# Performance work log

Measured on AMD Instinct MI355X. Metric: run time of the kernel, lower is better.

## Reference

```python
import jax, jax.numpy as jnp
import numpy as np

B, S, DIN, DOUT = 2, 2048, 4096, 4096


def setup_inputs() -> dict:
    key = jax.random.key(0)
    k1, k2 = jax.random.split(key)
    x = jax.random.normal(k1, (B, S, DIN), dtype=jnp.float32)
    weight = jax.random.normal(k2, (DOUT, DIN), dtype=jnp.float32) * 0.02
    # xnor init for row scaling pattern
    mean = weight.mean(-1, keepdims=True)                      # [DOUT,1]
    scale = jnp.abs(weight - mean).mean(-1, keepdims=True)     # [DOUT,1]
    wscale = scale
    wbias = mean
    return {"x": x, "weight": weight, "wscale": wscale, "wbias": wbias}


def reference(x, weight, wscale, wbias):
    # STE binarization: forward = sign(weight) (grad handled in bwd module)
    w_bin = jnp.sign(weight)
    w = wscale * w_bin + wbias                                 # [DOUT, DIN]
    # F.linear(x, w): x @ w.T, no bias
    out = jnp.einsum('bsk,nk->bsn', x, w)
    return out
```

## Files before the change

kernel.cpp:

```cpp
#include <hip/hip_runtime.h>
#include <stdint.h>


#define MDIM 4096
#define NDIM 4096
#define KDIM 4096

typedef int int4v  __attribute__((ext_vector_type(4)));

__device__ __forceinline__ int pack4_rn(float a, float b, float c, float d, float inv) {
  int ia = __float2int_rn(a * inv) & 0xff;
  int ib = __float2int_rn(b * inv) & 0xff;
  int ic = __float2int_rn(c * inv) & 0xff;
  int id = __float2int_rn(d * inv) & 0xff;
  return ia | (ib << 8) | (ic << 16) | (id << 24);
}

__device__ __forceinline__ int sgn8(float v) {
  return (v > 0.f) ? 1 : ((v < 0.f) ? 0xff : 0);
}

#define PREP_XB 1024
#define PREP_WB 1024
__global__ __launch_bounds__(256) void prep_kernel(
    const float* __restrict__ x, const float* __restrict__ w,
    char* __restrict__ xq, char* __restrict__ wsg,
    float* __restrict__ xscale, float* __restrict__ sumx) {
  const int b = blockIdx.x;
  const int tid = threadIdx.x;
  const int lane = tid & 63, wv = tid >> 6;
  if (b < PREP_XB) {
    const int row = b * 4 + wv;
    const float4* xr = (const float4*)(x + (size_t)row * KDIM);
    float4 v[16];
    float s = 0.f, amax = 0.f;
#pragma unroll
    for (int u = 0; u < 16; ++u) {
      v[u] = xr[u * 64 + lane];
      s += v[u].x + v[u].y + v[u].z + v[u].w;
      amax = fmaxf(amax, fmaxf(fmaxf(fabsf(v[u].x), fabsf(v[u].y)),
                               fmaxf(fabsf(v[u].z), fabsf(v[u].w))));
    }
#pragma unroll
    for (int off = 32; off > 0; off >>= 1) {
      s += __shfl_xor(s, off, 64);
      amax = fmaxf(amax, __shfl_xor(amax, off, 64));
    }
    if (lane == 0) {
      sumx[row] = s;
      xscale[row] = amax * (1.f / 127.f);
    }
    const float inv = (amax > 0.f) ? 127.f / amax : 0.f;
    int* xo = (int*)(xq + (size_t)row * KDIM);
#pragma unroll
    for (int u = 0; u < 16; ++u)
      xo[u * 64 + lane] = pack4_rn(v[u].x, v[u].y, v[u].z, v[u].w, inv);
  } else {
    const float4* wr = (const float4*)w;
    int* wo = (int*)wsg;
    const size_t i0 = (size_t)(b - PREP_XB) * 256 + tid;
    const size_t stride = (size_t)PREP_WB * 256;
#pragma unroll
    for (int u = 0; u < 16; ++u) {
      size_t i = i0 + (size_t)u * stride;
      float4 vv = wr[i];
      wo[i] = sgn8(vv.x) | (sgn8(vv.y) << 8) | (sgn8(vv.z) << 16) | (sgn8(vv.w) << 24);
    }
  }
}

__global__ __launch_bounds__(512, 2) void gemm_bin_i8_pipe(
    const char* __restrict__ A, const char* __restrict__ Bs,
    const float* __restrict__ wscale, const float* __restrict__ wbias,
    const float* __restrict__ xscale, const float* __restrict__ sumx,
    float* __restrict__ C) {
  __shared__ __align__(16) char sm[131072];

  const int bm = blockIdx.x >> 4, bn = blockIdx.x & 15;
  const int tm0 = bm * 256, tn0 = bn * 256;
  const int tid = threadIdx.x;
  const int lane = tid & 63, wave = tid >> 6;
  const int col32 = lane & 31, hl = lane >> 5;
  const int wr = wave >> 2, wc = wave & 3;

  typedef int int16v __attribute__((ext_vector_type(16)));
  int16v acc[4][2];
#pragma unroll
  for (int mi = 0; mi < 4; ++mi)
#pragma unroll
    for (int nj = 0; nj < 2; ++nj)
#pragma unroll
      for (int r = 0; r < 16; ++r) acc[mi][nj][r] = 0;

  int4v afA[4], bqA[2], afB[4], bqB[2];

  int aOff[2][4], bOff[2][2];
#pragma unroll
  for (int ks2 = 0; ks2 < 2; ++ks2) {
#pragma unroll
    for (int mi = 0; mi < 4; ++mi) {
      int row = wr * 128 + mi * 32 + col32;
      int sw = (row >> 1) & 3;
      aOff[ks2][mi] = row * 64 + (((ks2 * 2 + hl) ^ sw) & 3) * 16;
    }
#pragma unroll
    for (int nj = 0; nj < 2; ++nj) {
      int row = wc * 64 + nj * 32 + col32;
      int sw = (row >> 1) & 3;
      bOff[ks2][nj] = 65536 + row * 64 + (((ks2 * 2 + hl) ^ sw) & 3) * 16;
    }
  }

  const int u0 = tid, u1 = tid + 512;
  const int r0 = u0 >> 2, r1 = u1 >> 2;
  const int c0 = (u0 & 3) ^ ((r0 >> 1) & 3);
  const int c1 = (u1 & 3) ^ ((r1 >> 1) & 3);
  const char* gA0 = A + (size_t)(tm0 + r0) * KDIM + c0 * 16;
  const char* gA1 = A + (size_t)(tm0 + r1) * KDIM + c1 * 16;
  const char* gB0 = Bs + (size_t)(tn0 + r0) * KDIM + c0 * 16;
  const char* gB1 = Bs + (size_t)(tn0 + r1) * KDIM + c1 * 16;
  const int ldsu0 = tid * 16, ldsu1 = 8192 + tid * 16;

#define STAGE_A(BUF, KH, KOFS)                                                    \
  do {                                                                            \
    const int base_ = ((BUF) * 2 + (KH)) * 16384;                                 \
    __builtin_amdgcn_global_load_lds(                                             \
        (const __attribute__((address_space(1))) void*)(gA0 + (KOFS)),            \
        (__attribute__((address_space(3))) void*)(sm + base_ + ldsu0), 16, 0, 0); \
    __builtin_amdgcn_global_load_lds(                                             \
        (const __attribute__((address_space(1))) void*)(gA1 + (KOFS)),            \
        (__attribute__((address_space(3))) void*)(sm + base_ + ldsu1), 16, 0, 0); \
  } while (0)

#define STAGE_B(BUF, KH, KOFS)                                                    \
  do {                                                                            \
    const int base_ = 65536 + ((BUF) * 2 + (KH)) * 16384;                         \
    __builtin_amdgcn_global_load_lds(                                             \
        (const __attribute__((address_space(1))) void*)(gB0 + (KOFS)),            \
        (__attribute__((address_space(3))) void*)(sm + base_ + ldsu0), 16, 0, 0); \
    __builtin_amdgcn_global_load_lds(                                             \
        (const __attribute__((address_space(1))) void*)(gB1 + (KOFS)),            \
        (__attribute__((address_space(3))) void*)(sm + base_ + ldsu1), 16, 0, 0); \
  } while (0)

#define DSRD(SET, BUF, KS, KS2)                                                   \
  do {                                                                            \
    _Pragma("unroll") for (int mi_ = 0; mi_ < 4; ++mi_)                           \
        af##SET[mi_] =                                                            \
            *(const int4v*)(sm + ((BUF) * 2 + (KS)) * 16384 + aOff[KS2][mi_]);    \
    _Pragma("unroll") for (int nj_ = 0; nj_ < 2; ++nj_)                           \
        bq##SET[nj_] =                                                            \
            *(const int4v*)(sm + ((BUF) * 2 + (KS)) * 16384 + bOff[KS2][nj_]);    \
  } while (0)

#define MFMA8(SET)                                                                \
  do {                                                                            \
    __builtin_amdgcn_s_setprio(1);                                                \
    _Pragma("unroll") for (int mi_ = 0; mi_ < 4; ++mi_)                           \
        _Pragma("unroll") for (int nj_ = 0; nj_ < 2; ++nj_)                       \
            acc[mi_][nj_] = __builtin_amdgcn_mfma_i32_32x32x32_i8(                \
                af##SET[mi_], bq##SET[nj_], acc[mi_][nj_], 0, 0, 0);              \
    __builtin_amdgcn_s_setprio(0);                                                \
  } while (0)

#define WAITL6                                                                    \
  do {                                                                            \
    asm volatile("s_waitcnt lgkmcnt(6)" ::: "memory");                            \
    __builtin_amdgcn_sched_barrier(0);                                            \
  } while (0)
#define WAITL0                                                                    \
  do {                                                                            \
    asm volatile("s_waitcnt lgkmcnt(0)" ::: "memory");                            \
    __builtin_amdgcn_sched_barrier(0);                                            \
  } while (0)

#define BARO __builtin_amdgcn_s_barrier()
#define CK6  asm volatile("s_waitcnt vmcnt(6)\n\ts_barrier" ::: "memory")
#define CK4  asm volatile("s_waitcnt vmcnt(4)\n\ts_barrier" ::: "memory")
#define CK0  asm volatile("s_waitcnt vmcnt(0)\n\ts_barrier" ::: "memory")

#define PHASEP(CSET, NSET, NBUF, NKS, NKS2, STAGEOP, ENDSYNC)                     \
  do {                                                                            \
    DSRD(NSET, NBUF, NKS, NKS2);                                                  \
    STAGEOP;                                                                      \
    WAITL6;                                                                       \
    MFMA8(CSET);                                                                  \
    ENDSYNC;                                                                      \
  } while (0)

#define TILE_MAIN(BUF, TAU)                                                       \
  do {                                                                            \
    PHASEP(A, B, BUF, 0, 1, STAGE_A((BUF) ^ 1, 1, ((TAU) + 1) * 128 + 64), BARO); \
    PHASEP(B, A, BUF, 1, 0, STAGE_B((BUF) ^ 1, 1, ((TAU) + 1) * 128 + 64), BARO); \
    PHASEP(A, B, BUF, 1, 1, STAGE_A(BUF, 0, ((TAU) + 2) * 128), CK6);             \
    PHASEP(B, A, (BUF) ^ 1, 0, 0, STAGE_B(BUF, 0, ((TAU) + 2) * 128), CK4);       \
  } while (0)

  STAGE_A(0, 0, 0);
  STAGE_B(0, 0, 0);
  STAGE_A(0, 1, 64);
  STAGE_B(0, 1, 64);
  STAGE_A(1, 0, 128);
  STAGE_B(1, 0, 128);
  CK4;
  DSRD(A, 0, 0, 0);

#pragma unroll 1
  for (int t = 0; t < 30; t += 2) {
    TILE_MAIN(0, t);
    TILE_MAIN(1, t + 1);
  }

  PHASEP(A, B, 0, 0, 1, STAGE_A(1, 1, 31 * 128 + 64), BARO);
  PHASEP(B, A, 0, 1, 0, STAGE_B(1, 1, 31 * 128 + 64), BARO);
  PHASEP(A, B, 0, 1, 1, (void)0, CK4);
  PHASEP(B, A, 1, 0, 0, (void)0, CK0);
  PHASEP(A, B, 1, 0, 1, (void)0, BARO);
  PHASEP(B, A, 1, 1, 0, (void)0, BARO);
  PHASEP(A, B, 1, 1, 1, (void)0, BARO);
  WAITL0;
  MFMA8(B);

#undef TILE_MAIN
#undef PHASEP
#undef BARO
#undef CK6
#undef CK4
#undef CK0
#undef WAITL6
#undef WAITL0
#undef MFMA8
#undef DSRD
#undef STAGE_A
#undef STAGE_B

  float wsv[2], wbv[2];
#pragma unroll
  for (int nj = 0; nj < 2; ++nj) {
    int n = tn0 + wc * 64 + nj * 32 + col32;
    wsv[nj] = wscale[n];
    wbv[nj] = wbias[n];
  }
#pragma unroll
  for (int mi = 0; mi < 4; ++mi) {
#pragma unroll
    for (int reg = 0; reg < 16; ++reg) {
      int m = tm0 + wr * 128 + mi * 32 + (reg & 3) + 8 * (reg >> 2) + 4 * hl;
      float xs = xscale[m];
      float sx = sumx[m];
      float* crow = C + (size_t)m * NDIM + tn0 + wc * 64 + col32;
#pragma unroll
      for (int nj = 0; nj < 2; ++nj)
        crow[nj * 32] = wsv[nj] * xs * (float)acc[mi][nj][reg] + wbv[nj] * sx;
    }
  }
}

extern "C" void kernel_launch(void* const* d_in, const int* in_sizes, int n_in,
                              void* d_out, int out_size, void* d_ws, size_t ws_size,
                              hipStream_t stream) {
  const float* x      = (const float*)d_in[0];
  const float* weight = (const float*)d_in[1];
  const float* wscale = (const float*)d_in[2];
  const float* wbias  = (const float*)d_in[3];
  float* out = (float*)d_out;

  char* xq  = (char*)d_ws;
  char* wsg = xq + (size_t)MDIM * KDIM;
  float* xscale = (float*)(wsg + (size_t)NDIM * KDIM);
  float* sumx   = xscale + MDIM;

  prep_kernel<<<PREP_XB + PREP_WB, 256, 0, stream>>>(
      x, weight, xq, wsg, xscale, sumx);
  gemm_bin_i8_pipe<<<(MDIM / 256) * (NDIM / 256), 512, 0, stream>>>(
      xq, wsg, wscale, wbias, xscale, sumx, out);
}
```

Baseline: 235.9 us.

## Coarsen GEMM pipeline phases to full 64-byte K slices with fused A/B staging

Restructures the int8 MFMA main loop so each phase reads a full 64-byte K half-tile (both 32-byte sub-steps) for A and B and issues 16 MFMAs, instead of 8 MFMAs per quarter phase. A and B global-to-LDS loads are combined into one staging step, and there are now two barriers per 128-K tile instead of four. LDS offsets are computed from a per-lane base plus constant strides, cutting register-held offset arrays. This lowers barrier and wait overhead per MFMA, at the cost of twice the fragment registers per set and less fine-grained overlap of loads with compute.

After: 242.6 us. 2.8% more time.

```diff
diff --git a/kernel.cpp b/kernel.cpp
--- a/kernel.cpp
+++ b/kernel.cpp
@@ -7,6 +7,7 @@
 #define KDIM 4096
 
 typedef int int4v  __attribute__((ext_vector_type(4)));
+typedef int int16v __attribute__((ext_vector_type(16)));
 
 __device__ __forceinline__ int pack4_rn(float a, float b, float c, float d, float inv) {
   int ia = __float2int_rn(a * inv) & 0xff;
@@ -69,7 +70,7 @@
   }
 }
 
-__global__ __launch_bounds__(512, 2) void gemm_bin_i8_pipe(
+__global__ __launch_bounds__(512, 2) void gemm_bin_i8_m2(
     const char* __restrict__ A, const char* __restrict__ Bs,
     const float* __restrict__ wscale, const float* __restrict__ wbias,
     const float* __restrict__ xscale, const float* __restrict__ sumx,
@@ -83,7 +84,6 @@
   const int col32 = lane & 31, hl = lane >> 5;
   const int wr = wave >> 2, wc = wave & 3;
 
-  typedef int int16v __attribute__((ext_vector_type(16)));
   int16v acc[4][2];
 #pragma unroll
   for (int mi = 0; mi < 4; ++mi)
@@ -92,80 +92,73 @@
 #pragma unroll
       for (int r = 0; r < 16; ++r) acc[mi][nj][r] = 0;
 
-  int4v afA[4], bqA[2], afB[4], bqB[2];
-
-  int aOff[2][4], bOff[2][2];
+  int4v afA[8], bqA[4], afB[8], bqB[4];
+
+  const int swc = (col32 >> 1) & 3;
+  int baseA[2], baseB[2];
 #pragma unroll
   for (int ks2 = 0; ks2 < 2; ++ks2) {
-#pragma unroll
-    for (int mi = 0; mi < 4; ++mi) {
-      int row = wr * 128 + mi * 32 + col32;
-      int sw = (row >> 1) & 3;
-      aOff[ks2][mi] = row * 64 + (((ks2 * 2 + hl) ^ sw) & 3) * 16;
-    }
-#pragma unroll
-    for (int nj = 0; nj < 2; ++nj) {
-      int row = wc * 64 + nj * 32 + col32;
-      int sw = (row >> 1) & 3;
-      bOff[ks2][nj] = 65536 + row * 64 + (((ks2 * 2 + hl) ^ sw) & 3) * 16;
-    }
+    baseA[ks2] = (wr * 128 + col32) * 64 + (((ks2 * 2 + hl) ^ swc) & 3) * 16;
+    baseB[ks2] = (wc * 64 + col32) * 64 + (((ks2 * 2 + hl) ^ swc) & 3) * 16;
   }
 
   const int u0 = tid, u1 = tid + 512;
   const int r0 = u0 >> 2, r1 = u1 >> 2;
   const int c0 = (u0 & 3) ^ ((r0 >> 1) & 3);
   const int c1 = (u1 & 3) ^ ((r1 >> 1) & 3);
-  const char* gA0 = A + (size_t)(tm0 + r0) * KDIM + c0 * 16;
-  const char* gA1 = A + (size_t)(tm0 + r1) * KDIM + c1 * 16;
-  const char* gB0 = Bs + (size_t)(tn0 + r0) * KDIM + c0 * 16;
-  const char* gB1 = Bs + (size_t)(tn0 + r1) * KDIM + c1 * 16;
+  const int offs0 = r0 * KDIM + c0 * 16;
+  const int offs1 = r1 * KDIM + c1 * 16;
+  const char* Abase = A + (size_t)tm0 * KDIM;
+  const char* Bbase = Bs + (size_t)tn0 * KDIM;
   const int ldsu0 = tid * 16, ldsu1 = 8192 + tid * 16;
 
-#define STAGE_A(BUF, KH, KOFS)                                                    \
-  do {                                                                            \
-    const int base_ = ((BUF) * 2 + (KH)) * 16384;                                 \
-    __builtin_amdgcn_global_load_lds(                                             \
-        (const __attribute__((address_space(1))) void*)(gA0 + (KOFS)),            \
-        (__attribute__((address_space(3))) void*)(sm + base_ + ldsu0), 16, 0, 0); \
-    __builtin_amdgcn_global_load_lds(                                             \
-        (const __attribute__((address_space(1))) void*)(gA1 + (KOFS)),            \
-        (__attribute__((address_space(3))) void*)(sm + base_ + ldsu1), 16, 0, 0); \
-  } while (0)
-
-#define STAGE_B(BUF, KH, KOFS)                                                    \
-  do {                                                                            \
-    const int base_ = 65536 + ((BUF) * 2 + (KH)) * 16384;                         \
-    __builtin_amdgcn_global_load_lds(                                             \
-        (const __attribute__((address_space(1))) void*)(gB0 + (KOFS)),            \
-        (__attribute__((address_space(3))) void*)(sm + base_ + ldsu0), 16, 0, 0); \
-    __builtin_amdgcn_global_load_lds(                                             \
-        (const __attribute__((address_space(1))) void*)(gB1 + (KOFS)),            \
-        (__attribute__((address_space(3))) void*)(sm + base_ + ldsu1), 16, 0, 0); \
-  } while (0)
-
-#define DSRD(SET, BUF, KS, KS2)                                                   \
-  do {                                                                            \
-    _Pragma("unroll") for (int mi_ = 0; mi_ < 4; ++mi_)                           \
-        af##SET[mi_] =                                                            \
-            *(const int4v*)(sm + ((BUF) * 2 + (KS)) * 16384 + aOff[KS2][mi_]);    \
-    _Pragma("unroll") for (int nj_ = 0; nj_ < 2; ++nj_)                           \
-        bq##SET[nj_] =                                                            \
-            *(const int4v*)(sm + ((BUF) * 2 + (KS)) * 16384 + bOff[KS2][nj_]);    \
-  } while (0)
-
-#define MFMA8(SET)                                                                \
+#define STAGE_AB(BUF, KH, KOFS)                                                   \
+  do {                                                                            \
+    const int sa_ = ((BUF) * 2 + (KH)) * 16384;                                   \
+    const int sb_ = 65536 + sa_;                                                  \
+    __builtin_amdgcn_global_load_lds(                                             \
+        (const __attribute__((address_space(1))) void*)(Abase + offs0 + (KOFS)),  \
+        (__attribute__((address_space(3))) void*)(sm + sa_ + ldsu0), 16, 0, 0);   \
+    __builtin_amdgcn_global_load_lds(                                             \
+        (const __attribute__((address_space(1))) void*)(Abase + offs1 + (KOFS)),  \
+        (__attribute__((address_space(3))) void*)(sm + sa_ + ldsu1), 16, 0, 0);   \
+    __builtin_amdgcn_global_load_lds(                                             \
+        (const __attribute__((address_space(1))) void*)(Bbase + offs0 + (KOFS)),  \
+        (__attribute__((address_space(3))) void*)(sm + sb_ + ldsu0), 16, 0, 0);   \
+    __builtin_amdgcn_global_load_lds(                                             \
+        (const __attribute__((address_space(1))) void*)(Bbase + offs1 + (KOFS)),  \
+        (__attribute__((address_space(3))) void*)(sm + sb_ + ldsu1), 16, 0, 0);   \
+  } while (0)
+
+#define DSRD(SET, BUF, KS)                                                        \
+  do {                                                                            \
+    const int sa_ = ((BUF) * 2 + (KS)) * 16384;                                   \
+    const int sb_ = 65536 + sa_;                                                  \
+    _Pragma("unroll") for (int k2_ = 0; k2_ < 2; ++k2_) {                         \
+      _Pragma("unroll") for (int mi_ = 0; mi_ < 4; ++mi_)                         \
+          af##SET[k2_ * 4 + mi_] =                                                \
+              *(const int4v*)(sm + sa_ + baseA[k2_] + mi_ * 2048);                \
+      _Pragma("unroll") for (int nj_ = 0; nj_ < 2; ++nj_)                         \
+          bq##SET[k2_ * 2 + nj_] =                                                \
+              *(const int4v*)(sm + sb_ + baseB[k2_] + nj_ * 2048);                \
+    }                                                                             \
+  } while (0)
+
+#define MFMA16(SET)                                                               \
   do {                                                                            \
     __builtin_amdgcn_s_setprio(1);                                                \
-    _Pragma("unroll") for (int mi_ = 0; mi_ < 4; ++mi_)                           \
-        _Pragma("unroll") for (int nj_ = 0; nj_ < 2; ++nj_)                       \
-            acc[mi_][nj_] = __builtin_amdgcn_mfma_i32_32x32x32_i8(                \
-                af##SET[mi_], bq##SET[nj_], acc[mi_][nj_], 0, 0, 0);              \
+    _Pragma("unroll") for (int k2_ = 0; k2_ < 2; ++k2_)                           \
+        _Pragma("unroll") for (int mi_ = 0; mi_ < 4; ++mi_)                       \
+            _Pragma("unroll") for (int nj_ = 0; nj_ < 2; ++nj_)                   \
+                acc[mi_][nj_] = __builtin_amdgcn_mfma_i32_32x32x32_i8(            \
+                    af##SET[k2_ * 4 + mi_], bq##SET[k2_ * 2 + nj_],               \
+                    acc[mi_][nj_], 0, 0, 0);                                      \
     __builtin_amdgcn_s_setprio(0);                                                \
   } while (0)
 
-#define WAITL6                                                                    \
-  do {                                                                            \
-    asm volatile("s_waitcnt lgkmcnt(6)" ::: "memory");                            \
+#define WAITL12                                                                   \
+  do {                                                                            \
+    asm volatile("s_waitcnt lgkmcnt(12)" ::: "memory");                           \
     __builtin_amdgcn_sched_barrier(0);                                            \
   } while (0)
 #define WAITL0                                                                    \
@@ -174,36 +167,29 @@
     __builtin_amdgcn_sched_barrier(0);                                            \
   } while (0)
 
-#define BARO __builtin_amdgcn_s_barrier()
-#define CK6  asm volatile("s_waitcnt vmcnt(6)\n\ts_barrier" ::: "memory")
-#define CK4  asm volatile("s_waitcnt vmcnt(4)\n\ts_barrier" ::: "memory")
-#define CK0  asm volatile("s_waitcnt vmcnt(0)\n\ts_barrier" ::: "memory")
-
-#define PHASEP(CSET, NSET, NBUF, NKS, NKS2, STAGEOP, ENDSYNC)                     \
-  do {                                                                            \
-    DSRD(NSET, NBUF, NKS, NKS2);                                                  \
+#define CKV4 asm volatile("s_waitcnt vmcnt(4)\n\ts_barrier" ::: "memory")
+#define CKV0 asm volatile("s_waitcnt vmcnt(0)\n\ts_barrier" ::: "memory")
+
+#define PHASE(CSET, NSET, NBUF, NKS, STAGEOP, ENDSYNC)                            \
+  do {                                                                            \
+    DSRD(NSET, NBUF, NKS);                                                        \
     STAGEOP;                                                                      \
-    WAITL6;                                                                       \
-    MFMA8(CSET);                                                                  \
+    WAITL12;                                                                      \
+    MFMA16(CSET);                                                                 \
     ENDSYNC;                                                                      \
   } while (0)
 
 #define TILE_MAIN(BUF, TAU)                                                       \
   do {                                                                            \
-    PHASEP(A, B, BUF, 0, 1, STAGE_A((BUF) ^ 1, 1, ((TAU) + 1) * 128 + 64), BARO); \
-    PHASEP(B, A, BUF, 1, 0, STAGE_B((BUF) ^ 1, 1, ((TAU) + 1) * 128 + 64), BARO); \
-    PHASEP(A, B, BUF, 1, 1, STAGE_A(BUF, 0, ((TAU) + 2) * 128), CK6);             \
-    PHASEP(B, A, (BUF) ^ 1, 0, 0, STAGE_B(BUF, 0, ((TAU) + 2) * 128), CK4);       \
-  } while (0)
-
-  STAGE_A(0, 0, 0);
-  STAGE_B(0, 0, 0);
-  STAGE_A(0, 1, 64);
-  STAGE_B(0, 1, 64);
-  STAGE_A(1, 0, 128);
-  STAGE_B(1, 0, 128);
-  CK4;
-  DSRD(A, 0, 0, 0);
+    PHASE(A, B, BUF, 1, STAGE_AB((BUF) ^ 1, 1, ((TAU) + 1) * 128 + 64), CKV4);    \
+    PHASE(B, A, (BUF) ^ 1, 0, STAGE_AB(BUF, 0, ((TAU) + 2) * 128), CKV4);         \
+  } while (0)
+
+  STAGE_AB(0, 0, 0);
+  STAGE_AB(0, 1, 64);
+  STAGE_AB(1, 0, 128);
+  CKV4;
+  DSRD(A, 0, 0);
 
 #pragma unroll 1
   for (int t = 0; t < 30; t += 2) {
@@ -211,28 +197,21 @@
     TILE_MAIN(1, t + 1);
   }
 
-  PHASEP(A, B, 0, 0, 1, STAGE_A(1, 1, 31 * 128 + 64), BARO);
-  PHASEP(B, A, 0, 1, 0, STAGE_B(1, 1, 31 * 128 + 64), BARO);
-  PHASEP(A, B, 0, 1, 1, (void)0, CK4);
-  PHASEP(B, A, 1, 0, 0, (void)0, CK0);
-  PHASEP(A, B, 1, 0, 1, (void)0, BARO);
-  PHASEP(B, A, 1, 1, 0, (void)0, BARO);
-  PHASEP(A, B, 1, 1, 1, (void)0, BARO);
+  PHASE(A, B, 0, 1, STAGE_AB(1, 1, 31 * 128 + 64), CKV4);
+  PHASE(B, A, 1, 0, (void)0, CKV0);
+  PHASE(A, B, 1, 1, (void)0, (void)0);
   WAITL0;
-  MFMA8(B);
+  MFMA16(B);
 
 #undef TILE_MAIN
-#undef PHASEP
-#undef BARO
-#undef CK6
-#undef CK4
-#undef CK0
-#undef WAITL6
+#undef PHASE
+#undef CKV4
+#undef CKV0
+#undef WAITL12
 #undef WAITL0
-#undef MFMA8
+#undef MFMA16
 #undef DSRD
-#undef STAGE_A
-#undef STAGE_B
+#undef STAGE_AB
 
   float wsv[2], wbv[2];
 #pragma unroll
@@ -272,6 +251,6 @@
 
   prep_kernel<<<PREP_XB + PREP_WB, 256, 0, stream>>>(
       x, weight, xq, wsg, xscale, sumx);
-  gemm_bin_i8_pipe<<<(MDIM / 256) * (NDIM / 256), 512, 0, stream>>>(
+  gemm_bin_i8_m2<<<(MDIM / 256) * (NDIM / 256), 512, 0, stream>>>(
       xq, wsg, wscale, wbias, xscale, sumx, out);
 }
```
